# Optimization experiments

Hardware: AMD Instinct MI355X
Metric: run time of the kernel (lower is better)

## Reference

```python
import jax, jax.numpy as jnp
import numpy as np

B, S, DIM, HD = 4, 1024, 2048, 128
H = DIM // HD  # 16 heads
GN_EPS = 1e-3  # Keras GroupNormalization default epsilon


def setup_inputs() -> dict:
    key = jax.random.key(0)
    ks = jax.random.split(key, 8)
    x = jax.random.normal(ks[0], (B, S, DIM), dtype=jnp.float32)
    k = jax.random.normal(ks[1], (B, S, DIM), dtype=jnp.float32)
    v = jax.random.normal(ks[2], (B, S, DIM), dtype=jnp.float32)
    # One shared QKV projection weight per head (dict.fromkeys bug in source
    # makes Q, K, V use the SAME Dense layer). Keras Dense: y = x @ W, W:(in,out)
    Wh = jax.random.normal(ks[3], (H, HD, HD), dtype=jnp.float32) / np.sqrt(HD)
    wg_w = jax.random.normal(ks[4], (DIM, DIM), dtype=jnp.float32) / np.sqrt(DIM)
    wo_w = jax.random.normal(ks[5], (DIM, DIM), dtype=jnp.float32) / np.sqrt(DIM)
    gn_gamma = jnp.ones((DIM,), dtype=jnp.float32)
    gn_beta = jnp.zeros((DIM,), dtype=jnp.float32)
    return {"x": x, "k": k, "v": v, "Wh": Wh, "wg_w": wg_w, "wo_w": wo_w,
            "gn_gamma": gn_gamma, "gn_beta": gn_beta}


def _decay_masks(n_heads, seq_len):
    # Source: band_part(gamma**(i-j), 0, -1) then transpose ->
    # D[h, i, j] = gamma_h ** (j - i) for j <= i, else 0.
    gam = 1.0 - 2.0 ** (-5.0 - jnp.arange(n_heads, dtype=jnp.float32))  # (H,)
    idx = jnp.arange(seq_len, dtype=jnp.float32)
    expo = idx[None, :] - idx[:, None]               # (S,S): j - i
    D = jnp.where(expo[None, :, :] <= 0,
                  gam[:, None, None] ** expo[None, :, :], 0.0)  # (H,S,S)
    # TF: D /= reduce_sum(D, 1)**0.5 broadcasts row-sums along the COLUMN axis
    return D / jnp.sqrt(D.sum(axis=-1))[:, None, :]


def reference(x, k, v, Wh, wg_w, wo_w, gn_gamma, gn_beta):
    b, s, dim = x.shape
    h, hd, _ = Wh.shape
    # split last axis into contiguous per-head chunks
    xh = x.reshape(b, s, h, hd)
    kh = k.reshape(b, s, h, hd)
    vh = v.reshape(b, s, h, hd)
    # Q, K, V share the same per-head weight (faithful to dict.fromkeys)
    Q = jnp.einsum('bshd,hde->bshe', xh, Wh)
    K = jnp.einsum('bshd,hde->bshe', kh, Wh)
    V = jnp.einsum('bshd,hde->bshe', vh, Wh)
    scores = jnp.einsum('bshe,bthe->bhst', Q, K) / jnp.sqrt(jnp.float32(hd))
    Dn = _decay_masks(h, s)                          # (H,S,S)
    masked = scores * Dn[None, :, :, :]              # (B,H,S,S)
    # source reduces over axis 0 == BATCH, then abs, then clamp at 1
    A = jnp.maximum(jnp.abs(masked.sum(axis=0)), 1.0)  # (H,S,S)
    O = jnp.einsum('hst,bthe->bshe', A, V).reshape(b, s, dim)
    # GroupNormalization(groups=1): per-token layernorm over channels
    mu = O.mean(axis=-1, keepdims=True)
    var = O.var(axis=-1, keepdims=True)
    Y = (O - mu) / jnp.sqrt(var + GN_EPS) * gn_gamma + gn_beta
    W = jax.nn.relu(x @ wg_w)                        # gated branch
    return (W * Y) @ wo_w
```

## Files before the change

kernel.cpp:

```cpp
#include <hip/hip_runtime.h>
#include <math.h>

constexpr int Bc = 4, Sc = 1024, Dc = 2048, HDc = 128, Hc = 16;
constexpr int BSc = Bc * Sc;
constexpr int KQKc = Bc * HDc;
#define GN_EPS 1e-3f

typedef __bf16 bf16x8 __attribute__((ext_vector_type(8)));
typedef __bf16 bf16x4 __attribute__((ext_vector_type(4)));
typedef float f32x4 __attribute__((ext_vector_type(4)));

constexpr size_t OFF_Q   = 0;
constexpr size_t OFF_K   = OFF_Q + (size_t)Hc * Sc * KQKc / 2;
constexpr size_t OFF_VB  = OFF_K + (size_t)Hc * Sc * KQKc / 2;
constexpr size_t OFF_VT  = OFF_VB + (size_t)BSc * Dc / 2;
constexpr size_t OFF_A   = OFF_VT + (size_t)BSc * Dc / 2;
constexpr size_t OFF_O   = OFF_A + (size_t)Hc * Sc * Sc / 2;
constexpr size_t OFF_CT  = OFF_O + (size_t)BSc * Dc;
constexpr size_t OFF_PN  = OFF_CT + (size_t)Hc * Sc;
constexpr size_t OFF_XB  = OFF_PN + (size_t)Hc * Sc;
constexpr size_t OFF_WGT = OFF_XB + (size_t)BSc * Dc / 2;
constexpr size_t OFF_WOT = OFF_WGT + (size_t)Dc * Dc / 2;
constexpr size_t OFF_SUF = OFF_WOT + (size_t)Dc * Dc / 2;
constexpr size_t OFF_T   = OFF_SUF + (size_t)64 * 9 * HDc;
constexpr size_t OFF_WHT = OFF_T + (size_t)64 * 8 * HDc;
constexpr size_t OFF_STAT= OFF_WHT + (size_t)Hc * HDc * HDc / 2;
constexpr size_t OFF_KB2 = OFF_A;
constexpr size_t OFF_VB2 = OFF_A + (size_t)BSc * Dc / 2;

#define GLOAD_LDS16(gp, lp)                                               \
  __builtin_amdgcn_global_load_lds(                                       \
      (const __attribute__((address_space(1))) void*)(gp),                \
      (__attribute__((address_space(3))) void*)(lp), 16, 0, 0)


constexpr int ABUFE = 128 * 64;
constexpr int BBUFE = 128 * 64;
constexpr int MG_LDS = (3 * ABUFE + 2 * BBUFE) * 2;
constexpr int PJ_LDS = 4 * 8192 * 2;

template <int ASTR, int BSTR, int NF = 4>
__device__ __forceinline__ void mfma_loop128(const __bf16* __restrict__ Abase,
                                             const __bf16* __restrict__ Bbase,
                                             const int ntk,
                                             __bf16* As, __bf16* Bs,
                                             const int wave, const int lane,
                                             f32x4 acc[4][4]) {
  constexpr int NH = NF / 2;
  const int wr = wave >> 1, wc = wave & 1;
  const int lr = lane >> 2;
  const int lkx = ((lane & 3) ^ ((lane >> 3) & 3)) * 8;
  const int rl = lane & 15, kq = lane >> 4;
  const int swo = rl * 32 + ((kq ^ ((rl >> 1) & 3)) * 8);

#define SA_(i, kt, bsel) do {                                               \
    const int ci_ = (i) * 4 + wave;                                         \
    GLOAD_LDS16(Abase + (size_t)((ci_ >> 1) * 16 + lr) * ASTR               \
                    + (kt) * 64 + (ci_ & 1) * 32 + lkx,                     \
                As + (bsel) * ABUFE + ci_ * 512);                           \
  } while (0)
#define SB_(j, kt, bsel) do {                                               \
    const int ci_ = (j) * 4 + wave;                                         \
    GLOAD_LDS16(Bbase + (size_t)((ci_ >> 1) * 16 + lr) * BSTR               \
                    + (kt) * 64 + (ci_ & 1) * 32 + lkx,                     \
                Bs + (bsel) * BBUFE + ci_ * 512);                           \
  } while (0)

  SA_(0, 0, 0); SA_(1, 0, 0); SA_(2, 0, 0); SA_(3, 0, 0);
  #pragma unroll
  for (int j = 0; j < NF; ++j) SB_(j, 0, 0);
  SA_(0, 1, 1); SA_(1, 1, 1); SA_(2, 1, 1); SA_(3, 1, 1);
  __builtin_amdgcn_sched_barrier(0);
  asm volatile("s_waitcnt vmcnt(4)" ::: "memory");
  __builtin_amdgcn_sched_barrier(0);
  __builtin_amdgcn_s_barrier();

  int cbA = 0;
  for (int t = 0; t < ntk; ++t) {
    const int sbA = (cbA + 2 >= 3) ? cbA - 1 : cbA + 2;
    const __bf16* Ac = As + cbA * ABUFE;
    const __bf16* Bc = Bs + (t & 1) * BBUFE;
    bf16x8 a[4][2], b[NF][2];
    #pragma unroll
    for (int m = 0; m < 2; ++m)
      #pragma unroll
      for (int kc = 0; kc < 2; ++kc)
        a[m][kc] = *(const bf16x8*)&Ac[((wr * 4 + m) * 2 + kc) * 512 + swo];
    #pragma unroll
    for (int n = 0; n < NH; ++n)
      #pragma unroll
      for (int kc = 0; kc < 2; ++kc)
        b[n][kc] = *(const bf16x8*)&Bc[((wc * NF + n) * 2 + kc) * 512 + swo];
    #pragma unroll
    for (int m = 2; m < 4; ++m)
      #pragma unroll
      for (int kc = 0; kc < 2; ++kc)
        a[m][kc] = *(const bf16x8*)&Ac[((wr * 4 + m) * 2 + kc) * 512 + swo];
    #pragma unroll
    for (int n = NH; n < NF; ++n)
      #pragma unroll
      for (int kc = 0; kc < 2; ++kc)
        b[n][kc] = *(const bf16x8*)&Bc[((wc * NF + n) * 2 + kc) * 512 + swo];
    if (t + 1 < ntk) {
      #pragma unroll
      for (int j = 0; j < NF; ++j) SB_(j, t + 1, (t + 1) & 1);
    }
    if (t + 2 < ntk) {
      SA_(0, t + 2, sbA); SA_(1, t + 2, sbA);
      SA_(2, t + 2, sbA); SA_(3, t + 2, sbA);
    }
    __builtin_amdgcn_sched_barrier(0);
    __builtin_amdgcn_s_setprio(1);
    #pragma unroll
    for (int kc = 0; kc < 2; ++kc)
      #pragma unroll
      for (int m = 0; m < 2; ++m)
        #pragma unroll
        for (int n = 0; n < NH; ++n)
          acc[m][n] = __builtin_amdgcn_mfma_f32_16x16x32_bf16(
              a[m][kc], b[n][kc], acc[m][n], 0, 0, 0);
    __builtin_amdgcn_s_setprio(0);
    __builtin_amdgcn_sched_barrier(0);
    __builtin_amdgcn_s_setprio(1);
    #pragma unroll
    for (int kc = 0; kc < 2; ++kc)
      #pragma unroll
      for (int m = 2; m < 4; ++m)
        #pragma unroll
        for (int n = 0; n < NH; ++n)
          acc[m][n] = __builtin_amdgcn_mfma_f32_16x16x32_bf16(
              a[m][kc], b[n][kc], acc[m][n], 0, 0, 0);
    __builtin_amdgcn_s_setprio(0);
    __builtin_amdgcn_sched_barrier(0);
    __builtin_amdgcn_s_setprio(1);
    #pragma unroll
    for (int kc = 0; kc < 2; ++kc)
      #pragma unroll
      for (int m = 0; m < 2; ++m)
        #pragma unroll
        for (int n = NH; n < NF; ++n)
          acc[m][n] = __builtin_amdgcn_mfma_f32_16x16x32_bf16(
              a[m][kc], b[n][kc], acc[m][n], 0, 0, 0);
    __builtin_amdgcn_s_setprio(0);
    __builtin_amdgcn_sched_barrier(0);
    __builtin_amdgcn_s_setprio(1);
    #pragma unroll
    for (int kc = 0; kc < 2; ++kc)
      #pragma unroll
      for (int m = 2; m < 4; ++m)
        #pragma unroll
        for (int n = NH; n < NF; ++n)
          acc[m][n] = __builtin_amdgcn_mfma_f32_16x16x32_bf16(
              a[m][kc], b[n][kc], acc[m][n], 0, 0, 0);
    __builtin_amdgcn_s_setprio(0);
    __builtin_amdgcn_sched_barrier(0);
    asm volatile("s_waitcnt lgkmcnt(0)" ::: "memory");
    __builtin_amdgcn_sched_barrier(0);
    if (t + 2 < ntk)
      asm volatile("s_waitcnt vmcnt(4)" ::: "memory");
    else if (t + 1 < ntk)
      asm volatile("s_waitcnt vmcnt(0)" ::: "memory");
    __builtin_amdgcn_sched_barrier(0);
    __builtin_amdgcn_s_barrier();
    cbA = (cbA + 1 >= 3) ? 0 : cbA + 1;
  }
#undef SA_
#undef SB_
}

__global__ __launch_bounds__(256) void k_tables(float* __restrict__ ct,
                                                float* __restrict__ pn,
                                                float* __restrict__ TP,
                                                float* __restrict__ STAT) {
  int idx = blockIdx.x * 256 + threadIdx.x;
  int h = idx >> 10, t = idx & 1023;
  double gamma = 1.0 - exp2(-(double)(5 + h));
  double l2g = log2(gamma);
  double r = 1.0 / gamma;
  double rowsum = (exp2(-(double)(t + 1) * l2g) - 1.0) / (r - 1.0);
  ct[idx] = (float)(exp2((double)t * l2g) / sqrt(rowsum));
  pn[idx] = (float)exp2(-(double)t * l2g);
  float4 z4 = {0.f, 0.f, 0.f, 0.f};
  *(float4*)(TP + (size_t)idx * 4) = z4;
  if (idx < BSc * 2) STAT[idx] = 0.f;
}

__global__ __launch_bounds__(256) void k_cast83(const float* __restrict__ s0,
                                                const float* __restrict__ s1,
                                                const float* __restrict__ s2,
                                                __bf16* __restrict__ d0,
                                                __bf16* __restrict__ d1,
                                                __bf16* __restrict__ d2) {
  const int y = blockIdx.y;
  const float* src = (y == 0) ? s0 : (y == 1) ? s1 : s2;
  __bf16* dst = (y == 0) ? d0 : (y == 1) ? d1 : d2;
  size_t i = ((size_t)blockIdx.x * 256 + threadIdx.x) * 8;
  float4 a = *(const float4*)(src + i);
  float4 b = *(const float4*)(src + i + 4);
  bf16x8 o;
  o[0] = (__bf16)a.x; o[1] = (__bf16)a.y; o[2] = (__bf16)a.z; o[3] = (__bf16)a.w;
  o[4] = (__bf16)b.x; o[5] = (__bf16)b.y; o[6] = (__bf16)b.z; o[7] = (__bf16)b.w;
  *(bf16x8*)(dst + i) = o;
}

__global__ __launch_bounds__(256) void k_castT2(const float* __restrict__ s0,
                                                const float* __restrict__ s1,
                                                __bf16* __restrict__ d0,
                                                __bf16* __restrict__ d1) {
  __shared__ float t[32][33];
  const int bx = blockIdx.x, by = blockIdx.y;
  const float* src = blockIdx.z ? s1 : s0;
  __bf16* dst = blockIdx.z ? d1 : d0;
  const int tid = threadIdx.x;
  const int lx = tid & 31, ly = tid >> 5;
  #pragma unroll
  for (int r = 0; r < 32; r += 8)
    t[ly + r][lx] = src[(size_t)(by * 32 + ly + r) * Dc + bx * 32 + lx];
  __syncthreads();
  #pragma unroll
  for (int r = 0; r < 32; r += 8)
    dst[(size_t)(bx * 32 + ly + r) * Dc + by * 32 + lx] = (__bf16)t[lx][ly + r];
}

__global__ __launch_bounds__(256) void k_whT(const float* __restrict__ Wh,
                                             __bf16* __restrict__ WhT) {
  __shared__ float t[32][33];
  const int h = blockIdx.z;
  const int d0 = blockIdx.x * 32, e0 = blockIdx.y * 32;
  const int tid = threadIdx.x;
  const int lx = tid & 31, ly = tid >> 5;
  #pragma unroll
  for (int r = 0; r < 32; r += 8)
    t[ly + r][lx] = Wh[(size_t)h * HDc * HDc + (d0 + ly + r) * HDc + e0 + lx];
  __syncthreads();
  #pragma unroll
  for (int r = 0; r < 32; r += 8)
    WhT[(size_t)h * HDc * HDc + (e0 + ly + r) * HDc + d0 + lx] =
        (__bf16)t[lx][ly + r];
}

__global__ __launch_bounds__(256, 2) void k_projm(const __bf16* __restrict__ Xb,
                                                  const __bf16* __restrict__ Kb2,
                                                  const __bf16* __restrict__ Vb2,
                                                  const __bf16* __restrict__ WhT,
                                                  __bf16* __restrict__ Qo,
                                                  __bf16* __restrict__ Ko,
                                                  __bf16* __restrict__ Vo) {
  extern __shared__ __bf16 lds[];
  __bf16* Xs = lds;
  __bf16* Ws = lds + 2 * 8192;
  const int r0 = blockIdx.x * 128;
  const int h = blockIdx.y;
  const int z = blockIdx.z;
  const __bf16* src = (z == 0) ? Xb : (z == 1) ? Kb2 : Vb2;
  const __bf16* wsrc = WhT + (size_t)h * HDc * HDc;
  const int tid = threadIdx.x;
  const int wave = tid >> 6, lane = tid & 63;
  const int wr = wave >> 1, wc = wave & 1;
  const int lr = lane >> 2;
  const int lkx = ((lane & 3) ^ ((lane >> 3) & 3)) * 8;
  const int rl = lane & 15, kq = lane >> 4;
  const int swo = rl * 32 + ((kq ^ ((rl >> 1) & 3)) * 8);
  #pragma unroll
  for (int kt = 0; kt < 2; ++kt) {
    #pragma unroll
    for (int i = 0; i < 4; ++i) {
      const int ci = i * 4 + wave;
      const int row = (ci >> 1) * 16 + lr;
      const int ko = kt * 64 + (ci & 1) * 32 + lkx;
      GLOAD_LDS16(src + (size_t)(r0 + row) * Dc + h * HDc + ko,
                  Xs + kt * 8192 + ci * 512);
      GLOAD_LDS16(wsrc + (size_t)row * HDc + ko, Ws + kt * 8192 + ci * 512);
    }
  }
  __builtin_amdgcn_sched_barrier(0);
  asm volatile("s_waitcnt vmcnt(0)" ::: "memory");
  __builtin_amdgcn_sched_barrier(0);
  __builtin_amdgcn_s_barrier();
  f32x4 acc[4][4] = {{}};
  #pragma unroll
  for (int kt = 0; kt < 2; ++kt) {
    bf16x8 a[4][2], b[4][2];
    #pragma unroll
    for (int m = 0; m < 4; ++m)
      #pragma unroll
      for (int kc = 0; kc < 2; ++kc)
        a[m][kc] =
            *(const bf16x8*)&Xs[kt * 8192 + ((wr * 4 + m) * 2 + kc) * 512 + swo];
    #pragma unroll
    for (int n = 0; n < 4; ++n)
      #pragma unroll
      for (int kc = 0; kc < 2; ++kc)
        b[n][kc] =
            *(const bf16x8*)&Ws[kt * 8192 + ((wc * 4 + n) * 2 + kc) * 512 + swo];
    #pragma unroll
    for (int kc = 0; kc < 2; ++kc)
      #pragma unroll
      for (int m = 0; m < 4; ++m)
        #pragma unroll
        for (int n = 0; n < 4; ++n)
          acc[m][n] = __builtin_amdgcn_mfma_f32_16x16x32_bf16(
              a[m][kc], b[n][kc], acc[m][n], 0, 0, 0);
  }
  #pragma unroll
  for (int mi = 0; mi < 4; ++mi) {
    #pragma unroll
    for (int nj = 0; nj < 4; ++nj) {
      const int col = wc * 64 + nj * 16 + rl;
      #pragma unroll
      for (int r = 0; r < 4; ++r) {
        const int row = r0 + wr * 64 + mi * 16 + kq * 4 + r;
        const __bf16 v = (__bf16)acc[mi][nj][r];
        if (z == 2) {
          Vo[(size_t)row * Dc + h * HDc + col] = v;
        } else {
          const int s = row & 1023, bb = row >> 10;
          __bf16* dst = (z == 0) ? Qo : Ko;
          dst[((size_t)(h * Sc + s) * Bc + bb) * HDc + col] = v;
        }
      }
    }
  }
}

__global__ __launch_bounds__(256) void k_vt(const __bf16* __restrict__ VB,
                                            __bf16* __restrict__ Vt,
                                            float* __restrict__ TP) {
  __shared__ float tl[32][33];
  __shared__ float rs[8][32];
  const int bh = blockIdx.z, bb = bh >> 4, h = bh & 15;
  const int t0 = blockIdx.x * 32, e0 = blockIdx.y * 32;
  const int tid = threadIdx.x;
  const int lx = tid & 31, ly = tid >> 5;
  float ps = 0.f;
  #pragma unroll
  for (int r = 0; r < 32; r += 8) {
    const float v =
        (float)VB[(size_t)(bb * Sc + t0 + ly + r) * Dc + h * HDc + e0 + lx];
    tl[ly + r][lx] = v;
    ps += v;
  }
  rs[ly][lx] = ps;
  __syncthreads();
  #pragma unroll
  for (int r = 0; r < 32; r += 8)
    Vt[((size_t)bh * HDc + e0 + ly + r) * Sc + t0 + lx] = (__bf16)tl[lx][ly + r];
  if (ly == 0) {
    float s = ((rs[0][lx] + rs[1][lx]) + (rs[2][lx] + rs[3][lx])) +
              ((rs[4][lx] + rs[5][lx]) + (rs[6][lx] + rs[7][lx]));
    atomicAdd(&TP[((size_t)bh * 8 + (t0 >> 7)) * HDc + e0 + lx], s);
  }
}

__global__ __launch_bounds__(128) void k_vscan(const float* __restrict__ T,
                                               float* __restrict__ SufV) {
  const int bh = blockIdx.x;
  const int e = threadIdx.x;
  float acc = 0.f;
  SufV[((size_t)bh * 9 + 8) * HDc + e] = 0.f;
  for (int jj = 7; jj >= 1; --jj) {
    acc += T[((size_t)bh * 8 + jj) * HDc + e];
    SufV[((size_t)bh * 9 + jj) * HDc + e] = acc;
  }
}

__global__ __launch_bounds__(256, 2) void k_ssm(const __bf16* __restrict__ Q,
                                                const __bf16* __restrict__ Kb,
                                                const float* __restrict__ ct,
                                                const float* __restrict__ pn,
                                                __bf16* __restrict__ A) {
  const int bx = blockIdx.x, by = blockIdx.y;
  int r, c, half;
  if (by == 8)       { r = bx; c = bx; half = 1; }
  else if (bx > by)  { r = bx; c = by; half = 1; }
  else               { r = by; c = bx; half = 0; }
  extern __shared__ __bf16 lds[];
  __bf16* As = lds;
  __bf16* Bs = lds + 3 * ABUFE;
  const int h = blockIdx.z;
  const int s0 = r * 128;
  const int t0 = c * 128 + half * 64;
  const int tid = threadIdx.x;
  __bf16* Ah = A + (size_t)h * Sc * Sc;
  const int wave = tid >> 6, lane = tid & 63;
  f32x4 acc[4][4] = {{}};
  mfma_loop128<KQKc, KQKc, 2>(Q + (size_t)(h * Sc + s0) * KQKc,
                              Kb + (size_t)(h * Sc + t0) * KQKc, KQKc / 64,
                              As, Bs, wave, lane, acc);
  const int wr = wave >> 1, wc = wave & 1;
  const int rl = lane & 15, kq = lane >> 4;
  const float rs = 0.088388347648318447f;
  #pragma unroll
  for (int mi = 0; mi < 4; ++mi) {
    #pragma unroll
    for (int nj = 0; nj < 2; ++nj) {
      const int t = t0 + wc * 32 + nj * 16 + rl;
      const float ctv = ct[h * Sc + t] * rs;
      #pragma unroll
      for (int rr = 0; rr < 4; ++rr) {
        const int s = s0 + wr * 64 + mi * 16 + kq * 4 + rr;
        float v = 1.0f;
        if (t <= s) v = fmaxf(fabsf(ctv * pn[h * Sc + s] * acc[mi][nj][rr]), 1.0f);
        Ah[(size_t)s * Sc + t] = (__bf16)v;
      }
    }
  }
}

__global__ __launch_bounds__(256, 2) void k_avm(const __bf16* __restrict__ A,
                                                const __bf16* __restrict__ Vt,
                                                const float* __restrict__ SufV,
                                                float* __restrict__ O,
                                                float* __restrict__ STAT) {
  extern __shared__ __bf16 lds[];
  __bf16* As = lds;
  __bf16* Bs = lds + 3 * ABUFE;
  const int lid = (int)blockIdx.z * 8 + (int)blockIdx.x;
  const int slot = lid & 255;
  const int bh = slot >> 2;
  const int itile = (lid < 256) ? (slot & 3) : 7 - (slot & 3);
  const int bb = bh >> 4, h = bh & 15;
  const int s0 = itile * 128;
  const int tid = threadIdx.x;
  const int wave = tid >> 6, lane = tid & 63;
  const int wr = wave >> 1, wc = wave & 1;
  const int rl = lane & 15, kq = lane >> 4;
  f32x4 acc[4][4] = {{}};
  mfma_loop128<Sc, Sc>(A + (size_t)(h * Sc + s0) * Sc,
                       Vt + (size_t)bh * HDc * Sc, (itile + 1) * 2, As, Bs,
                       wave, lane, acc);
  const float* sufr = SufV + ((size_t)bh * 9 + (itile + 1)) * HDc;
  #pragma unroll
  for (int mi = 0; mi < 4; ++mi) {
    #pragma unroll
    for (int r = 0; r < 4; ++r) {
      const int s = s0 + wr * 64 + mi * 16 + kq * 4 + r;
      const size_t orow = (size_t)(bb * Sc + s);
      float vs = 0.f, vq = 0.f;
      #pragma unroll
      for (int nj = 0; nj < 4; ++nj) {
        const int e = wc * 64 + nj * 16 + rl;
        const float v = acc[mi][nj][r] + sufr[e];
        O[orow * Dc + h * HDc + e] = v;
        vs += v;
        vq += v * v;
      }
      #pragma unroll
      for (int m = 1; m < 16; m <<= 1) {
        vs += __shfl_xor(vs, m);
        vq += __shfl_xor(vq, m);
      }
      if (rl == 0) {
        atomicAdd(&STAT[orow * 2], vs);
        atomicAdd(&STAT[orow * 2 + 1], vq);
      }
    }
  }
}

__global__ __launch_bounds__(256, 2) void k_mgemm(const __bf16* __restrict__ Ab,
                                                  const __bf16* __restrict__ Bt,
                                                  const float* __restrict__ Y,
                                                  const float* __restrict__ gw,
                                                  const float* __restrict__ bw,
                                                  const float* __restrict__ STAT,
                                                  __bf16* __restrict__ Gout,
                                                  float* __restrict__ Fout,
                                                  int mode) {
  extern __shared__ __bf16 lds[];
  __bf16* As = lds;
  __bf16* Bs = lds + 3 * ABUFE;
  int wid = blockIdx.y * gridDim.x + blockIdx.x;
  wid = (wid & 7) * 64 + (wid >> 3);
  const int r0 = (wid >> 4) * 128;
  const int c0 = (wid & 15) * 128;
  const int tid = threadIdx.x;
  const int wave = tid >> 6, lane = tid & 63;
  f32x4 acc[4][4] = {{}};
  mfma_loop128<Dc, Dc>(Ab + (size_t)r0 * Dc, Bt + (size_t)c0 * Dc, Dc / 64,
                       As, Bs, wave, lane, acc);
  const int wr = wave >> 1, wc = wave & 1;
  const int rl = lane & 15, kq = lane >> 4;
  if (mode == 0) {
    #pragma unroll
    for (int mi = 0; mi < 4; ++mi) {
      #pragma unroll
      for (int r = 0; r < 4; ++r) {
        const int row = r0 + wr * 64 + mi * 16 + kq * 4 + r;
        const float mu = STAT[(size_t)row * 2] * (1.0f / Dc);
        const float va = STAT[(size_t)row * 2 + 1] * (1.0f / Dc) - mu * mu;
        const float inv = rsqrtf(va + GN_EPS);
        #pragma unroll
        for (int nj = 0; nj < 4; ++nj) {
          const int col = c0 + wc * 64 + nj * 16 + rl;
          const size_t idx = (size_t)row * Dc + col;
          const float yv = (Y[idx] - mu) * inv * gw[col] + bw[col];
          Gout[idx] = (__bf16)(fmaxf(acc[mi][nj][r], 0.f) * yv);
        }
      }
    }
  } else {
    #pragma unroll
    for (int mi = 0; mi < 4; ++mi) {
      #pragma unroll
      for (int nj = 0; nj < 4; ++nj) {
        const int col = c0 + wc * 64 + nj * 16 + rl;
        #pragma unroll
        for (int r = 0; r < 4; ++r) {
          const int row = r0 + wr * 64 + mi * 16 + kq * 4 + r;
          Fout[(size_t)row * Dc + col] = acc[mi][nj][r];
        }
      }
    }
  }
}

extern "C" void kernel_launch(void* const* d_in, const int* in_sizes, int n_in,
                              void* d_out, int out_size, void* d_ws, size_t ws_size,
                              hipStream_t stream) {
  const float* x  = (const float*)d_in[0];
  const float* k  = (const float*)d_in[1];
  const float* v  = (const float*)d_in[2];
  const float* Wh = (const float*)d_in[3];
  const float* wg = (const float*)d_in[4];
  const float* wo = (const float*)d_in[5];
  const float* gg = (const float*)d_in[6];
  const float* gb = (const float*)d_in[7];
  float* ws = (float*)d_ws;
  __bf16* Q   = (__bf16*)(ws + OFF_Q);
  __bf16* Kp  = (__bf16*)(ws + OFF_K);
  __bf16* VB  = (__bf16*)(ws + OFF_VB);
  __bf16* Vt  = (__bf16*)(ws + OFF_VT);
  __bf16* A   = (__bf16*)(ws + OFF_A);
  float*  O   = ws + OFF_O;
  float*  CT  = ws + OFF_CT;
  float*  PN  = ws + OFF_PN;
  __bf16* XB  = (__bf16*)(ws + OFF_XB);
  __bf16* WGT = (__bf16*)(ws + OFF_WGT);
  __bf16* WOT = (__bf16*)(ws + OFF_WOT);
  float*  SUF = ws + OFF_SUF;
  float*  TP  = ws + OFF_T;
  __bf16* WHT = (__bf16*)(ws + OFF_WHT);
  float*  STAT= ws + OFF_STAT;
  __bf16* KB2 = (__bf16*)(ws + OFF_KB2);
  __bf16* VB2 = (__bf16*)(ws + OFF_VB2);
  __bf16* G   = (__bf16*)(ws + OFF_Q);

  static bool attr_done = false;
  if (!attr_done) {
    (void)hipFuncSetAttribute((const void*)k_mgemm,
                              hipFuncAttributeMaxDynamicSharedMemorySize,
                              MG_LDS);
    (void)hipFuncSetAttribute((const void*)k_projm,
                              hipFuncAttributeMaxDynamicSharedMemorySize,
                              PJ_LDS);
    (void)hipFuncSetAttribute((const void*)k_ssm,
                              hipFuncAttributeMaxDynamicSharedMemorySize,
                              MG_LDS);
    (void)hipFuncSetAttribute((const void*)k_avm,
                              hipFuncAttributeMaxDynamicSharedMemorySize,
                              MG_LDS);
    attr_done = true;
  }

  k_tables<<<Hc * Sc / 256, 256, 0, stream>>>(CT, PN, TP, STAT);
  k_cast83<<<dim3((BSc * Dc) / (256 * 8), 3), 256, 0, stream>>>(
      x, k, v, XB, KB2, VB2);
  k_castT2<<<dim3(Dc / 32, Dc / 32, 2), 256, 0, stream>>>(wg, wo, WGT, WOT);
  k_whT<<<dim3(4, 4, Hc), 256, 0, stream>>>(Wh, WHT);
  k_projm<<<dim3(BSc / 128, Hc, 3), 256, PJ_LDS, stream>>>(XB, KB2, VB2, WHT,
                                                           Q, Kp, VB);
  k_vt<<<dim3(Sc / 32, HDc / 32, Bc * Hc), 256, 0, stream>>>(VB, Vt, TP);
  k_vscan<<<Bc * Hc, 128, 0, stream>>>(TP, SUF);
  k_ssm<<<dim3(8, 9, Hc), 256, MG_LDS, stream>>>(Q, Kp, CT, PN, A);
  k_avm<<<dim3(8, 1, Bc * Hc), 256, MG_LDS, stream>>>(A, Vt, SUF, O, STAT);
  k_mgemm<<<dim3(16, 32), 256, MG_LDS, stream>>>(XB, WGT, O, gg, gb, STAT, G,
                                                 nullptr, 0);
  k_mgemm<<<dim3(16, 32), 256, MG_LDS, stream>>>(G, WOT, nullptr, nullptr,
                                                 nullptr, nullptr, nullptr,
                                                 (float*)d_out, 1);
}
```

Before: 348.5 us.

## Split A·V tiles into 64-row halves, pairing short and long causal segments per block

The MFMA GEMM loop now takes the M-fragment count as a template parameter, so the A operand tile can be 64 rows instead of 128. k_avm now processes two 64-row segments per block, pairing a short causal tile with its complementary long one (j and 7-j, opposite halves) to balance work across blocks. Its LDS footprint drops accordingly. The aim is better load balance and lower LDS/register use for the triangular A·V product. In exchange, B-tile reuse per loaded V chunk is halved and each block runs two pipeline prologues serially.

```diff
diff --git a/kernel.cpp b/kernel.cpp
--- a/kernel.cpp
+++ b/kernel.cpp
@@ -38,26 +38,37 @@
 constexpr int BBUFE = 128 * 64;
 constexpr int MG_LDS = (3 * ABUFE + 2 * BBUFE) * 2;
 constexpr int PJ_LDS = 4 * 8192 * 2;
-
-template <int ASTR, int BSTR, int NF = 4>
+constexpr int AV_LDS = (3 * 64 * 64 + 2 * BBUFE) * 2;
+
+template <int ASTR, int BSTR, int NF = 4, int MF = 4>
 __device__ __forceinline__ void mfma_loop128(const __bf16* __restrict__ Abase,
                                              const __bf16* __restrict__ Bbase,
                                              const int ntk,
                                              __bf16* As, __bf16* Bs,
                                              const int wave, const int lane,
-                                             f32x4 acc[4][4]) {
+                                             f32x4 acc[MF][NF]) {
   constexpr int NH = NF / 2;
+  constexpr int MH = MF / 2;
+  constexpr int ABE = MF * 2048;
   const int wr = wave >> 1, wc = wave & 1;
   const int lr = lane >> 2;
   const int lkx = ((lane & 3) ^ ((lane >> 3) & 3)) * 8;
   const int rl = lane & 15, kq = lane >> 4;
   const int swo = rl * 32 + ((kq ^ ((rl >> 1) & 3)) * 8);
 
+#define VMW_MF()                                                            \
+  do {                                                                      \
+    if constexpr (MF == 4)                                                  \
+      asm volatile("s_waitcnt vmcnt(4)" ::: "memory");                      \
+    else                                                                    \
+      asm volatile("s_waitcnt vmcnt(2)" ::: "memory");                      \
+  } while (0)
+
 #define SA_(i, kt, bsel) do {                                               \
     const int ci_ = (i) * 4 + wave;                                         \
     GLOAD_LDS16(Abase + (size_t)((ci_ >> 1) * 16 + lr) * ASTR               \
                     + (kt) * 64 + (ci_ & 1) * 32 + lkx,                     \
-                As + (bsel) * ABUFE + ci_ * 512);                           \
+                As + (bsel) * ABE + ci_ * 512);                             \
   } while (0)
 #define SB_(j, kt, bsel) do {                                               \
     const int ci_ = (j) * 4 + wave;                                         \
@@ -66,36 +77,38 @@
                 Bs + (bsel) * BBUFE + ci_ * 512);                           \
   } while (0)
 
-  SA_(0, 0, 0); SA_(1, 0, 0); SA_(2, 0, 0); SA_(3, 0, 0);
+  #pragma unroll
+  for (int i = 0; i < MF; ++i) SA_(i, 0, 0);
   #pragma unroll
   for (int j = 0; j < NF; ++j) SB_(j, 0, 0);
-  SA_(0, 1, 1); SA_(1, 1, 1); SA_(2, 1, 1); SA_(3, 1, 1);
+  #pragma unroll
+  for (int i = 0; i < MF; ++i) SA_(i, 1, 1);
   __builtin_amdgcn_sched_barrier(0);
-  asm volatile("s_waitcnt vmcnt(4)" ::: "memory");
+  VMW_MF();
   __builtin_amdgcn_sched_barrier(0);
   __builtin_amdgcn_s_barrier();
 
   int cbA = 0;
   for (int t = 0; t < ntk; ++t) {
     const int sbA = (cbA + 2 >= 3) ? cbA - 1 : cbA + 2;
-    const __bf16* Ac = As + cbA * ABUFE;
+    const __bf16* Ac = As + cbA * ABE;
     const __bf16* Bc = Bs + (t & 1) * BBUFE;
-    bf16x8 a[4][2], b[NF][2];
-    #pragma unroll
-    for (int m = 0; m < 2; ++m)
+    bf16x8 a[MF][2], b[NF][2];
+    #pragma unroll
+    for (int m = 0; m < MH; ++m)
       #pragma unroll
       for (int kc = 0; kc < 2; ++kc)
-        a[m][kc] = *(const bf16x8*)&Ac[((wr * 4 + m) * 2 + kc) * 512 + swo];
+        a[m][kc] = *(const bf16x8*)&Ac[((wr * MF + m) * 2 + kc) * 512 + swo];
     #pragma unroll
     for (int n = 0; n < NH; ++n)
       #pragma unroll
       for (int kc = 0; kc < 2; ++kc)
         b[n][kc] = *(const bf16x8*)&Bc[((wc * NF + n) * 2 + kc) * 512 + swo];
     #pragma unroll
-    for (int m = 2; m < 4; ++m)
+    for (int m = MH; m < MF; ++m)
       #pragma unroll
       for (int kc = 0; kc < 2; ++kc)
-        a[m][kc] = *(const bf16x8*)&Ac[((wr * 4 + m) * 2 + kc) * 512 + swo];
+        a[m][kc] = *(const bf16x8*)&Ac[((wr * MF + m) * 2 + kc) * 512 + swo];
     #pragma unroll
     for (int n = NH; n < NF; ++n)
       #pragma unroll
@@ -106,15 +119,15 @@
       for (int j = 0; j < NF; ++j) SB_(j, t + 1, (t + 1) & 1);
     }
     if (t + 2 < ntk) {
-      SA_(0, t + 2, sbA); SA_(1, t + 2, sbA);
-      SA_(2, t + 2, sbA); SA_(3, t + 2, sbA);
+      #pragma unroll
+      for (int i = 0; i < MF; ++i) SA_(i, t + 2, sbA);
     }
     __builtin_amdgcn_sched_barrier(0);
     __builtin_amdgcn_s_setprio(1);
     #pragma unroll
     for (int kc = 0; kc < 2; ++kc)
       #pragma unroll
-      for (int m = 0; m < 2; ++m)
+      for (int m = 0; m < MH; ++m)
         #pragma unroll
         for (int n = 0; n < NH; ++n)
           acc[m][n] = __builtin_amdgcn_mfma_f32_16x16x32_bf16(
@@ -125,7 +138,7 @@
     #pragma unroll
     for (int kc = 0; kc < 2; ++kc)
       #pragma unroll
-      for (int m = 2; m < 4; ++m)
+      for (int m = MH; m < MF; ++m)
         #pragma unroll
         for (int n = 0; n < NH; ++n)
           acc[m][n] = __builtin_amdgcn_mfma_f32_16x16x32_bf16(
@@ -136,7 +149,7 @@
     #pragma unroll
     for (int kc = 0; kc < 2; ++kc)
       #pragma unroll
-      for (int m = 0; m < 2; ++m)
+      for (int m = 0; m < MH; ++m)
         #pragma unroll
         for (int n = NH; n < NF; ++n)
           acc[m][n] = __builtin_amdgcn_mfma_f32_16x16x32_bf16(
@@ -147,7 +160,7 @@
     #pragma unroll
     for (int kc = 0; kc < 2; ++kc)
       #pragma unroll
-      for (int m = 2; m < 4; ++m)
+      for (int m = MH; m < MF; ++m)
         #pragma unroll
         for (int n = NH; n < NF; ++n)
           acc[m][n] = __builtin_amdgcn_mfma_f32_16x16x32_bf16(
@@ -156,16 +169,18 @@
     __builtin_amdgcn_sched_barrier(0);
     asm volatile("s_waitcnt lgkmcnt(0)" ::: "memory");
     __builtin_amdgcn_sched_barrier(0);
-    if (t + 2 < ntk)
-      asm volatile("s_waitcnt vmcnt(4)" ::: "memory");
-    else if (t + 1 < ntk)
+    if (t + 2 < ntk) {
+      VMW_MF();
+    } else if (t + 1 < ntk) {
       asm volatile("s_waitcnt vmcnt(0)" ::: "memory");
+    }
     __builtin_amdgcn_sched_barrier(0);
     __builtin_amdgcn_s_barrier();
     cbA = (cbA + 1 >= 3) ? 0 : cbA + 1;
   }
 #undef SA_
 #undef SB_
+#undef VMW_MF
 }
 
 __global__ __launch_bounds__(256) void k_tables(float* __restrict__ ct,
@@ -383,7 +398,7 @@
   const int tid = threadIdx.x;
   __bf16* Ah = A + (size_t)h * Sc * Sc;
   const int wave = tid >> 6, lane = tid & 63;
-  f32x4 acc[4][4] = {{}};
+  f32x4 acc[4][2] = {{}};
   mfma_loop128<KQKc, KQKc, 2>(Q + (size_t)(h * Sc + s0) * KQKc,
                               Kb + (size_t)(h * Sc + t0) * KQKc, KQKc / 64,
                               As, Bs, wave, lane, acc);
@@ -414,45 +429,48 @@
                                                 float* __restrict__ STAT) {
   extern __shared__ __bf16 lds[];
   __bf16* As = lds;
-  __bf16* Bs = lds + 3 * ABUFE;
-  const int lid = (int)blockIdx.z * 8 + (int)blockIdx.x;
-  const int slot = lid & 255;
-  const int bh = slot >> 2;
-  const int itile = (lid < 256) ? (slot & 3) : 7 - (slot & 3);
-  const int bb = bh >> 4, h = bh & 15;
-  const int s0 = itile * 128;
+  __bf16* Bs = lds + 3 * 64 * 64;
+  const int bh = blockIdx.z, bb = bh >> 4, h = bh & 15;
+  const int j = (int)blockIdx.x >> 1;
+  const int hh0 = (int)blockIdx.x & 1;
   const int tid = threadIdx.x;
   const int wave = tid >> 6, lane = tid & 63;
   const int wr = wave >> 1, wc = wave & 1;
   const int rl = lane & 15, kq = lane >> 4;
-  f32x4 acc[4][4] = {{}};
-  mfma_loop128<Sc, Sc>(A + (size_t)(h * Sc + s0) * Sc,
-                       Vt + (size_t)bh * HDc * Sc, (itile + 1) * 2, As, Bs,
-                       wave, lane, acc);
-  const float* sufr = SufV + ((size_t)bh * 9 + (itile + 1)) * HDc;
-  #pragma unroll
-  for (int mi = 0; mi < 4; ++mi) {
-    #pragma unroll
-    for (int r = 0; r < 4; ++r) {
-      const int s = s0 + wr * 64 + mi * 16 + kq * 4 + r;
-      const size_t orow = (size_t)(bb * Sc + s);
-      float vs = 0.f, vq = 0.f;
-      #pragma unroll
-      for (int nj = 0; nj < 4; ++nj) {
-        const int e = wc * 64 + nj * 16 + rl;
-        const float v = acc[mi][nj][r] + sufr[e];
-        O[orow * Dc + h * HDc + e] = v;
-        vs += v;
-        vq += v * v;
-      }
-      #pragma unroll
-      for (int m = 1; m < 16; m <<= 1) {
-        vs += __shfl_xor(vs, m);
-        vq += __shfl_xor(vq, m);
-      }
-      if (rl == 0) {
-        atomicAdd(&STAT[orow * 2], vs);
-        atomicAdd(&STAT[orow * 2 + 1], vq);
+  #pragma unroll
+  for (int seg = 0; seg < 2; ++seg) {
+    const int itile = seg ? 7 - j : j;
+    const int hh = seg ? 1 - hh0 : hh0;
+    const int s0 = itile * 128 + hh * 64;
+    f32x4 acc[2][4] = {{}};
+    mfma_loop128<Sc, Sc, 4, 2>(A + (size_t)(h * Sc + s0) * Sc,
+                               Vt + (size_t)bh * HDc * Sc, (itile + 1) * 2,
+                               As, Bs, wave, lane, acc);
+    const float* sufr = SufV + ((size_t)bh * 9 + (itile + 1)) * HDc;
+    #pragma unroll
+    for (int mi = 0; mi < 2; ++mi) {
+      #pragma unroll
+      for (int r = 0; r < 4; ++r) {
+        const int s = s0 + wr * 32 + mi * 16 + kq * 4 + r;
+        const size_t orow = (size_t)(bb * Sc + s);
+        float vs = 0.f, vq = 0.f;
+        #pragma unroll
+        for (int nj = 0; nj < 4; ++nj) {
+          const int e = wc * 64 + nj * 16 + rl;
+          const float v = acc[mi][nj][r] + sufr[e];
+          O[orow * Dc + h * HDc + e] = v;
+          vs += v;
+          vq += v * v;
+        }
+        #pragma unroll
+        for (int m = 1; m < 16; m <<= 1) {
+          vs += __shfl_xor(vs, m);
+          vq += __shfl_xor(vq, m);
+        }
+        if (rl == 0) {
+          atomicAdd(&STAT[orow * 2], vs);
+          atomicAdd(&STAT[orow * 2 + 1], vq);
+        }
       }
     }
   }
@@ -559,7 +577,7 @@
                               MG_LDS);
     (void)hipFuncSetAttribute((const void*)k_avm,
                               hipFuncAttributeMaxDynamicSharedMemorySize,
-                              MG_LDS);
+                              AV_LDS);
     attr_done = true;
   }
 
@@ -573,7 +591,7 @@
   k_vt<<<dim3(Sc / 32, HDc / 32, Bc * Hc), 256, 0, stream>>>(VB, Vt, TP);
   k_vscan<<<Bc * Hc, 128, 0, stream>>>(TP, SUF);
   k_ssm<<<dim3(8, 9, Hc), 256, MG_LDS, stream>>>(Q, Kp, CT, PN, A);
-  k_avm<<<dim3(8, 1, Bc * Hc), 256, MG_LDS, stream>>>(A, Vt, SUF, O, STAT);
+  k_avm<<<dim3(8, 1, Bc * Hc), 256, AV_LDS, stream>>>(A, Vt, SUF, O, STAT);
   k_mgemm<<<dim3(16, 32), 256, MG_LDS, stream>>>(XB, WGT, O, gg, gb, STAT, G,
                                                  nullptr, 0);
   k_mgemm<<<dim3(16, 32), 256, MG_LDS, stream>>>(G, WOT, nullptr, nullptr,
```

After: 365.2 us. 4.8% more time.
